# Kernel optimization log

Hardware: AMD Instinct MI355X
Metric: run time of the kernel (lower is better)

The kernel has to match this reference:

```python
import jax, jax.numpy as jnp
import numpy as np

N_NODES = 50000
N_EDGES = 800000
N_GRAPHS = 64
HEADS = 4
IN_CH, HID_CH, OUT_CH = 128, 64, 32


def setup_inputs() -> dict:
    key = jax.random.key(0)
    ks = jax.random.split(key, 13)
    x = jax.random.normal(ks[0], (N_NODES, IN_CH), dtype=jnp.float32)
    edge_index = jax.random.randint(ks[1], (2, N_EDGES), 0, N_NODES, dtype=jnp.int64)
    tensor_batch = jnp.sort(jax.random.randint(ks[2], (N_NODES,), 0, N_GRAPHS, dtype=jnp.int64))
    s = 0.1
    return {
        "x": x,
        "edge_index": edge_index,
        "tensor_batch": tensor_batch,
        "W1": jax.random.normal(ks[3], (IN_CH, HEADS * HID_CH), dtype=jnp.float32) * s,
        "a_src1": jax.random.normal(ks[4], (HEADS, HID_CH), dtype=jnp.float32) * s,
        "a_dst1": jax.random.normal(ks[5], (HEADS, HID_CH), dtype=jnp.float32) * s,
        "b1": jnp.zeros((HEADS * HID_CH,), dtype=jnp.float32),
        "W2": jax.random.normal(ks[6], (HEADS * HID_CH, HEADS * OUT_CH), dtype=jnp.float32) * s,
        "a_src2": jax.random.normal(ks[7], (HEADS, OUT_CH), dtype=jnp.float32) * s,
        "a_dst2": jax.random.normal(ks[8], (HEADS, OUT_CH), dtype=jnp.float32) * s,
        "b2": jnp.zeros((HEADS * OUT_CH,), dtype=jnp.float32),
        "Wout": jax.random.normal(ks[9], (HEADS * OUT_CH, 2), dtype=jnp.float32) * s,
        "bout": jnp.zeros((2,), dtype=jnp.float32),
    }


def gat_conv(x, src, dst, W, a_src, a_dst, b, heads, ch):
    """PyG-style GATConv (eval mode, self-loops already appended)."""
    N = x.shape[0]
    h = (x @ W).reshape(N, heads, ch)            # [N,H,C] per-head projection
    s = jnp.sum(h * a_src, axis=-1)              # [N,H] source attention term
    d = jnp.sum(h * a_dst, axis=-1)              # [N,H] dest attention term
    e = jax.nn.leaky_relu(s[src] + d[dst], negative_slope=0.2)   # [E,H]
    # segment softmax over incoming edges of each destination node
    m = jax.ops.segment_max(e, dst, num_segments=N)              # [N,H]
    ex = jnp.exp(e - m[dst])
    denom = jax.ops.segment_sum(ex, dst, num_segments=N)         # [N,H]
    alpha = ex / (denom[dst] + 1e-16)                            # [E,H]
    out = jax.ops.segment_sum(h[src] * alpha[:, :, None], dst, num_segments=N)
    return out.reshape(N, heads * ch) + b


def reference(x, edge_index, tensor_batch, W1, a_src1, a_dst1, b1,
              W2, a_src2, a_dst2, b2, Wout, bout):
    N = x.shape[0]
    loop = jnp.arange(N, dtype=edge_index.dtype)
    src = jnp.concatenate([edge_index[0], loop])  # add self-loops (PyG default)
    dst = jnp.concatenate([edge_index[1], loop])
    h = jax.nn.relu(gat_conv(x, src, dst, W1, a_src1, a_dst1, b1, HEADS, HID_CH))
    h = jax.nn.relu(gat_conv(h, src, dst, W2, a_src2, a_dst2, b2, HEADS, OUT_CH))
    # global mean pool per graph
    sums = jax.ops.segment_sum(h, tensor_batch, num_segments=N_GRAPHS)
    counts = jax.ops.segment_sum(jnp.ones((N, 1), h.dtype), tensor_batch, num_segments=N_GRAPHS)
    pooled = sums / jnp.maximum(counts, 1.0)
    logits = pooled @ Wout + bout
    return jax.nn.softmax(logits, axis=-1)
```

## Files before the change

### kernel.cpp

```cpp
#include <hip/hip_runtime.h>
#include <hip/hip_bf16.h>

#define N_NODES 50000
#define N_EDGES 800000
#define N_GRAPHS 64
#define HEADS 4
#define IN_CH 128
#define HID 64
#define F1 256
#define OUT_CH 32
#define F2 128
#define POOL_SPLITS 16
#define SCAN_B 256
#define SCAN_NB ((N_NODES + SCAN_B - 1) / SCAN_B)
#define GEMM_GRID ((N_NODES + 127) / 128)
#define COUNT_GRID ((N_EDGES + 255) / 256)

typedef unsigned short ushortT;
typedef unsigned int uintT;
typedef short v8s __attribute__((ext_vector_type(8)));
typedef float v4f __attribute__((ext_vector_type(4)));

__device__ __forceinline__ ushortT f2bf(float f) {
    union { float f; unsigned int i; } v; v.f = f;
    unsigned int x = v.i;
    unsigned int r = (x + 0x7fffu + ((x >> 16) & 1u)) >> 16;
    return (ushortT)r;
}
__device__ __forceinline__ float bf_lo(uintT w) {
    union { unsigned int i; float f; } v; v.i = w << 16; return v.f;
}
__device__ __forceinline__ float bf_hi(uintT w) {
    union { unsigned int i; float f; } v; v.i = w & 0xffff0000u; return v.f;
}

template <int FIN, int FOUT, bool ABF16>
__device__ __forceinline__ void gemm_body(const void* __restrict__ A,
                                          const float* __restrict__ W,
                                          const float* __restrict__ ASrc,
                                          const float* __restrict__ ADst,
                                          ushortT* __restrict__ out,
                                          float* __restrict__ s_out_g,
                                          float* __restrict__ d_out_g,
                                          int nrows, int bid) {
    constexpr int KC = FIN / 32;
    constexpr int NT = FOUT / 16;
    constexpr int NTH = (FOUT / HEADS) / 16;
    __shared__ uintT lW[FIN * FOUT / 2];
    int tid = threadIdx.x;
    constexpr int NQ = FIN * FOUT / 8;
    for (int i = tid; i < NQ; i += 256) {
        int lane = i & 63, g = i >> 6;
        int kc = g % KC, nt = g / KC;
        int n = nt * 16 + (lane & 15);
        int kbase = kc * 32 + (lane >> 4) * 8;
        union { uint4 q; ushortT u[8]; } pk;
#pragma unroll
        for (int j = 0; j < 8; j++) pk.u[j] = f2bf(W[(kbase + j) * FOUT + n]);
        ((uint4*)lW)[i] = pk.q;
    }
    __syncthreads();

    int wave = tid >> 6, lane = tid & 63;
    long rowA = (long)bid * 128 + wave * 32;
    long rowB = rowA + 16;
    bool doA = rowA < nrows, doB = rowB < nrows;
    if (!doA) return;
    int m = lane & 15, b = lane >> 4;

    v8s afA[KC], afB[KC];
    if (ABF16) {
        const ushortT* Ab = (const ushortT*)A;
#pragma unroll
        for (int kc = 0; kc < KC; kc++) {
            union { v8s v; uint4 q; } u;
            u.q = *(const uint4*)(Ab + (rowA + m) * FIN + kc * 32 + b * 8);
            afA[kc] = u.v;
            if (doB) {
                u.q = *(const uint4*)(Ab + (rowB + m) * FIN + kc * 32 + b * 8);
                afB[kc] = u.v;
            }
        }
    } else {
        const float* Af = (const float*)A;
#pragma unroll
        for (int kc = 0; kc < KC; kc++) {
            union { v8s v; ushortT u[8]; } u;
            const float* p = Af + (rowA + m) * FIN + kc * 32 + b * 8;
#pragma unroll
            for (int j = 0; j < 8; j++) u.u[j] = f2bf(p[j]);
            afA[kc] = u.v;
            if (doB) {
                const float* q = Af + (rowB + m) * FIN + kc * 32 + b * 8;
#pragma unroll
                for (int j = 0; j < 8; j++) u.u[j] = f2bf(q[j]);
                afB[kc] = u.v;
            }
        }
    }

    float spA[4] = {0,0,0,0}, dpA[4] = {0,0,0,0};
    float spB[4] = {0,0,0,0}, dpB[4] = {0,0,0,0};
    float skA[4], dkA[4], skB[4], dkB[4];
    const ushortT* lWs = (const ushortT*)lW;
#pragma unroll
    for (int nt = 0; nt < NT; nt++) {
        v4f cA = {0.f, 0.f, 0.f, 0.f}, cB = {0.f, 0.f, 0.f, 0.f};
#pragma unroll
        for (int kc = 0; kc < KC; kc++) {
            union { v8s v; uint4 q; } bu;
            bu.q = *(const uint4*)(lWs + ((nt * KC + kc) * 64 + lane) * 8);
            cA = __builtin_amdgcn_mfma_f32_16x16x32_bf16(afA[kc], bu.v, cA, 0, 0, 0);
            if (doB)
                cB = __builtin_amdgcn_mfma_f32_16x16x32_bf16(afB[kc], bu.v, cB, 0, 0, 0);
        }
        int col = nt * 16 + m;
        float av = ASrc[col], dv = ADst[col];
        long rA = rowA + b * 4;
#pragma unroll
        for (int reg = 0; reg < 4; reg++) {
            out[(rA + reg) * FOUT + col] = f2bf(cA[reg]);
            spA[reg] += cA[reg] * av;
            dpA[reg] += cA[reg] * dv;
        }
        if (doB) {
            long rB = rowB + b * 4;
#pragma unroll
            for (int reg = 0; reg < 4; reg++) {
                out[(rB + reg) * FOUT + col] = f2bf(cB[reg]);
                spB[reg] += cB[reg] * av;
                dpB[reg] += cB[reg] * dv;
            }
        }
        if ((nt % NTH) == NTH - 1) {
#pragma unroll
            for (int o = 1; o < 16; o <<= 1) {
#pragma unroll
                for (int reg = 0; reg < 4; reg++) {
                    spA[reg] += __shfl_xor(spA[reg], o, 64);
                    dpA[reg] += __shfl_xor(dpA[reg], o, 64);
                    spB[reg] += __shfl_xor(spB[reg], o, 64);
                    dpB[reg] += __shfl_xor(dpB[reg], o, 64);
                }
            }
            int hd = nt / NTH;
#pragma unroll
            for (int reg = 0; reg < 4; reg++) {
                if (m == hd) {
                    skA[reg] = spA[reg]; dkA[reg] = dpA[reg];
                    skB[reg] = spB[reg]; dkB[reg] = dpB[reg];
                }
                spA[reg] = 0.f; dpA[reg] = 0.f;
                spB[reg] = 0.f; dpB[reg] = 0.f;
            }
        }
    }
    if (m < HEADS) {
        long rA = rowA + b * 4;
#pragma unroll
        for (int reg = 0; reg < 4; reg++) {
            s_out_g[(rA + reg) * HEADS + m] = skA[reg];
            d_out_g[(rA + reg) * HEADS + m] = dkA[reg];
        }
        if (doB) {
            long rB = rowB + b * 4;
#pragma unroll
            for (int reg = 0; reg < 4; reg++) {
                s_out_g[(rB + reg) * HEADS + m] = skB[reg];
                d_out_g[(rB + reg) * HEADS + m] = dkB[reg];
            }
        }
    }
}

__global__ __launch_bounds__(256) void k_mega1(
        const float* __restrict__ x, const float* __restrict__ W1,
        const float* __restrict__ asrc1, const float* __restrict__ adst1,
        ushortT* __restrict__ u_h, float* __restrict__ f_s, float* __restrict__ f_d,
        const int* __restrict__ ei, int* __restrict__ counts,
        int* __restrict__ rank) {
    if (blockIdx.x < GEMM_GRID) {
        gemm_body<IN_CH, F1, false>(x, W1, asrc1, adst1, u_h, f_s, f_d,
                                    N_NODES, blockIdx.x);
    } else {
        int e = (blockIdx.x - GEMM_GRID) * 256 + threadIdx.x;
        if (e < N_EDGES) {
            int dst = ei[N_EDGES + e];
            rank[e] = atomicAdd(&counts[dst], 1);
        }
    }
}

__global__ __launch_bounds__(256) void k_gemm2(
        const ushortT* __restrict__ A, const float* __restrict__ W2,
        const float* __restrict__ asrc2, const float* __restrict__ adst2,
        ushortT* __restrict__ u_h, float* __restrict__ f_s, float* __restrict__ f_d) {
    gemm_body<F1, F2, true>(A, W2, asrc2, adst2, u_h, f_s, f_d,
                            N_NODES, blockIdx.x);
}

__global__ void k_scan1(const int* __restrict__ counts, int* __restrict__ offs,
                        int* __restrict__ bsum) {
    __shared__ int sh[SCAN_B];
    int b = blockIdx.x, t = threadIdx.x;
    int i = b * SCAN_B + t;
    int v = (i < N_NODES) ? counts[i] : 0;
    sh[t] = v;
    __syncthreads();
    for (int o = 1; o < SCAN_B; o <<= 1) {
        int add = (t >= o) ? sh[t - o] : 0;
        __syncthreads();
        sh[t] += add;
        __syncthreads();
    }
    if (i < N_NODES) offs[i] = sh[t] - v;
    if (t == SCAN_B - 1) bsum[b] = sh[t];
}

__global__ void k_scan2(const int* __restrict__ bsum, int* __restrict__ bbase,
                        int* __restrict__ offs, const int* __restrict__ batch,
                        int* __restrict__ bounds) {
    __shared__ int sh[SCAN_B];
    int t = threadIdx.x;
    int v = (t < SCAN_NB) ? bsum[t] : 0;
    sh[t] = v;
    __syncthreads();
    for (int o = 1; o < SCAN_B; o <<= 1) {
        int add = (t >= o) ? sh[t - o] : 0;
        __syncthreads();
        sh[t] += add;
        __syncthreads();
    }
    if (t < SCAN_NB) bbase[t] = sh[t] - v;
    if (t == SCAN_B - 1) offs[N_NODES] = sh[t];
    if (t <= N_GRAPHS) {
        int lo = 0, hi = N_NODES;
        while (lo < hi) {
            int mid = (lo + hi) >> 1;
            if (batch[mid] < t) lo = mid + 1; else hi = mid;
        }
        bounds[t] = lo;
    }
}

__global__ void k_scatter(const int* __restrict__ ei, const int* __restrict__ offs,
                          const int* __restrict__ bbase, const int* __restrict__ rank,
                          int* __restrict__ csr_src) {
    int e = blockIdx.x * blockDim.x + threadIdx.x;
    if (e >= N_EDGES) return;
    int src = ei[e], dst = ei[N_EDGES + e];
    int pos = offs[dst] + bbase[dst >> 8] + rank[e];
    csr_src[pos] = src;
}

template <int H, int C, int VEC, bool OUT_BF16, int WPB, int CHUNK>
__global__ __launch_bounds__(64 * WPB) void k_agg(
        const ushortT* __restrict__ hb, const float* __restrict__ s,
        const float* __restrict__ d, const int* __restrict__ offs,
        const int* __restrict__ bbase, const int* __restrict__ csr_src,
        const float* __restrict__ bias, void* __restrict__ xout) {
    static_assert(H == 4, "H=4 assumed");
    constexpr int F = H * C;
    constexpr int TPN = F / VEC;
    static_assert(TPN == 64, "one wave per node");
    __shared__ int lsrc[WPB][CHUNK];
    __shared__ float lex[WPB][CHUNK * H];
    int wv = threadIdx.x >> 6;
    int n = blockIdx.x * WPB + wv;
    if (n >= N_NODES) return;
    int t = threadIdx.x & 63;
    int h = t / (C / VEC);
    int beg = offs[n] + bbase[n >> 8];
    int np1 = n + 1;
    int end = (np1 < N_NODES) ? offs[np1] + bbase[np1 >> 8] : offs[N_NODES];
    float4 dn = *(const float4*)(d + n * 4);

    const uint2* hb2 = (const uint2*)hb;
    const uintT* hb1 = (const uintT*)hb;

    float4 svn = *(const float4*)(s + n * 4);
    float ssel = (h == 0) ? svn.x : (h == 1) ? svn.y : (h == 2) ? svn.z : svn.w;
    float dsel = (h == 0) ? dn.x : (h == 1) ? dn.y : (h == 2) ? dn.z : dn.w;
    float es = ssel + dsel; es = es > 0.f ? es : 0.2f * es;
    float exs = __expf(es);
    float sumex = exs;
    float acc[VEC];
    if (VEC == 4) {
        uint2 w = hb2[(long)n * TPN + t];
        acc[0] = exs * bf_lo(w.x); acc[1] = exs * bf_hi(w.x);
        acc[2] = exs * bf_lo(w.y); acc[3] = exs * bf_hi(w.y);
    } else {
        uintT w = hb1[(long)n * TPN + t];
        acc[0] = exs * bf_lo(w); acc[1] = exs * bf_hi(w);
    }

    for (int base = beg; base < end; base += CHUNK) {
        int cnt = min(CHUNK, end - base);
        for (int i = t; i < cnt; i += 64) {
            int sn = csr_src[base + i];
            lsrc[wv][i] = sn;
            float4 sv = *(const float4*)(s + sn * 4);
            float e0 = sv.x + dn.x; e0 = e0 > 0.f ? e0 : 0.2f * e0;
            float e1 = sv.y + dn.y; e1 = e1 > 0.f ? e1 : 0.2f * e1;
            float e2 = sv.z + dn.z; e2 = e2 > 0.f ? e2 : 0.2f * e2;
            float e3 = sv.w + dn.w; e3 = e3 > 0.f ? e3 : 0.2f * e3;
            float4 exv = { __expf(e0), __expf(e1), __expf(e2), __expf(e3) };
            *(float4*)&lex[wv][i * 4] = exv;
        }
        asm volatile("s_waitcnt lgkmcnt(0)" ::: "memory");
#pragma unroll 4
        for (int i = 0; i < cnt; i++) {
            float ex = lex[wv][i * H + h];
            int sn = lsrc[wv][i];
            sumex += ex;
            if (VEC == 4) {
                uint2 w = hb2[(long)sn * TPN + t];
                acc[0] += ex * bf_lo(w.x);
                acc[1] += ex * bf_hi(w.x);
                acc[2] += ex * bf_lo(w.y);
                acc[3] += ex * bf_hi(w.y);
            } else {
                uintT w = hb1[(long)sn * TPN + t];
                acc[0] += ex * bf_lo(w);
                acc[1] += ex * bf_hi(w);
            }
        }
        asm volatile("" ::: "memory");
    }
    float inv = 1.f / (sumex + 1e-16f);
    float o[VEC];
#pragma unroll
    for (int j = 0; j < VEC; j++)
        o[j] = fmaxf(acc[j] * inv + bias[t * VEC + j], 0.f);
    if (OUT_BF16) {
        if (VEC == 4) {
            uint2 pk;
            pk.x = (uintT)f2bf(o[0]) | ((uintT)f2bf(o[1]) << 16);
            pk.y = (uintT)f2bf(o[2]) | ((uintT)f2bf(o[3]) << 16);
            ((uint2*)xout)[(long)n * TPN + t] = pk;
        } else {
            uintT pk = (uintT)f2bf(o[0]) | ((uintT)f2bf(o[1]) << 16);
            ((uintT*)xout)[(long)n * TPN + t] = pk;
        }
    } else {
        float* xo = (float*)xout;
#pragma unroll
        for (int j = 0; j < VEC; j++) xo[(long)n * F + t * VEC + j] = o[j];
    }
}

__global__ void k_pool_partial(const ushortT* __restrict__ x2, const int* __restrict__ bounds,
                               float* __restrict__ partial) {
    int g = blockIdx.x, s = blockIdx.y;
    int t = threadIdx.x;
    int n0 = bounds[g], n1 = bounds[g + 1];
    int len = n1 - n0;
    int a = n0 + (int)((long)len * s / POOL_SPLITS);
    int b = n0 + (int)((long)len * (s + 1) / POOL_SPLITS);
    float acc = 0.f;
    for (int n = a; n < b; n++) acc += bf_lo((uintT)x2[(long)n * F2 + t]);
    partial[((long)g * POOL_SPLITS + s) * F2 + t] = acc;
}

__global__ void k_head(const float* __restrict__ partial, const int* __restrict__ bounds,
                       const float* __restrict__ Wout, const float* __restrict__ bout,
                       float* __restrict__ out) {
    __shared__ float red0[F2], red1[F2];
    int g = blockIdx.x;
    int t = threadIdx.x;
    int cntN = bounds[g + 1] - bounds[g];
    float cnt = fmaxf((float)cntN, 1.0f);
    float sum = 0.f;
    for (int s = 0; s < POOL_SPLITS; s++)
        sum += partial[((long)g * POOL_SPLITS + s) * F2 + t];
    float p = sum / cnt;
    red0[t] = p * Wout[t * 2 + 0];
    red1[t] = p * Wout[t * 2 + 1];
    __syncthreads();
    for (int off = F2 / 2; off > 0; off >>= 1) {
        if (t < off) { red0[t] += red0[t + off]; red1[t] += red1[t + off]; }
        __syncthreads();
    }
    if (t == 0) {
        float l0 = red0[0] + bout[0];
        float l1 = red1[0] + bout[1];
        float m = fmaxf(l0, l1);
        float e0 = __expf(l0 - m), e1 = __expf(l1 - m);
        float inv = 1.f / (e0 + e1);
        out[g * 2 + 0] = e0 * inv;
        out[g * 2 + 1] = e1 * inv;
    }
}

extern "C" void kernel_launch(void* const* d_in, const int* in_sizes, int n_in,
                              void* d_out, int out_size, void* d_ws, size_t ws_size,
                              hipStream_t stream) {
    const float* x     = (const float*)d_in[0];
    const int*   ei    = (const int*)d_in[1];
    const int*   batch = (const int*)d_in[2];
    const float* W1    = (const float*)d_in[3];
    const float* asrc1 = (const float*)d_in[4];
    const float* adst1 = (const float*)d_in[5];
    const float* b1    = (const float*)d_in[6];
    const float* W2    = (const float*)d_in[7];
    const float* asrc2 = (const float*)d_in[8];
    const float* adst2 = (const float*)d_in[9];
    const float* b2    = (const float*)d_in[10];
    const float* Wout  = (const float*)d_in[11];
    const float* bout  = (const float*)d_in[12];

    char* ws = (char*)d_ws;
    size_t off = 0;
    auto alloc = [&](size_t bytes) -> void* {
        void* p = ws + off;
        off += (bytes + 255) / 256 * 256;
        return p;
    };
    ushortT* u_h   = (ushortT*)alloc(sizeof(ushortT) * (size_t)N_NODES * F1);
    ushortT* u_x1  = (ushortT*)alloc(sizeof(ushortT) * (size_t)N_NODES * F1);
    ushortT* u_x2  = (ushortT*)alloc(sizeof(ushortT) * (size_t)N_NODES * F2);
    float*   f_s   = (float*)alloc(sizeof(float) * (size_t)N_NODES * HEADS);
    float*   f_d   = (float*)alloc(sizeof(float) * (size_t)N_NODES * HEADS);
    int*     i_cnt = (int*)alloc(sizeof(int) * (size_t)N_NODES);
    int*     i_off = (int*)alloc(sizeof(int) * (size_t)(N_NODES + 1));
    int*     i_rnk = (int*)alloc(sizeof(int) * (size_t)N_EDGES);
    int*     i_csr = (int*)alloc(sizeof(int) * (size_t)N_EDGES);
    int*     i_bnd = (int*)alloc(sizeof(int) * (size_t)(N_GRAPHS + 1));
    int*     i_bs  = (int*)alloc(sizeof(int) * SCAN_NB);
    int*     i_bb  = (int*)alloc(sizeof(int) * SCAN_NB);
    float*   f_prt = (float*)alloc(sizeof(float) * (size_t)N_GRAPHS * POOL_SPLITS * F2);
    (void)ws_size; (void)in_sizes; (void)n_in; (void)out_size;

    hipMemsetAsync(i_cnt, 0, sizeof(int) * N_NODES, stream);

    k_mega1<<<GEMM_GRID + COUNT_GRID, 256, 0, stream>>>(
        x, W1, asrc1, adst1, u_h, f_s, f_d, ei, i_cnt, i_rnk);

    k_scan1<<<SCAN_NB, SCAN_B, 0, stream>>>(i_cnt, i_off, i_bs);
    k_scan2<<<1, SCAN_B, 0, stream>>>(i_bs, i_bb, i_off, batch, i_bnd);
    k_scatter<<<COUNT_GRID, 256, 0, stream>>>(ei, i_off, i_bb, i_rnk, i_csr);

    int agg_grid = (N_NODES + 3) / 4;

    k_agg<HEADS, HID, 4, true, 4, 128><<<agg_grid, 256, 0, stream>>>(
        u_h, f_s, f_d, i_off, i_bb, i_csr, b1, u_x1);

    k_gemm2<<<GEMM_GRID, 256, 0, stream>>>(u_x1, W2, asrc2, adst2, u_h, f_s, f_d);
    k_agg<HEADS, OUT_CH, 2, true, 4, 128><<<agg_grid, 256, 0, stream>>>(
        u_h, f_s, f_d, i_off, i_bb, i_csr, b2, u_x2);

    dim3 pgrid(N_GRAPHS, POOL_SPLITS);
    k_pool_partial<<<pgrid, F2, 0, stream>>>(u_x2, i_bnd, f_prt);
    k_head<<<N_GRAPHS, F2, 0, stream>>>(f_prt, i_bnd, Wout, bout, (float*)d_out);
}
```

Baseline: 294.6 us.

## Store projected features in fp8 and prepack weights and input to bf16

The GEMMs now write the projected node features h as fp8 instead of bf16, which halves the bytes the edge aggregation kernels gather per neighbour. A new pre-pass kernel converts x to bf16 and packs W1/W2 into the MFMA layout once, so GEMM blocks only copy prepacked weights into LDS. This lowers precision of the gathered features and adds an extra kernel launch plus a write and re-read of a bf16 copy of x.

```diff
diff --git a/kernel.cpp b/kernel.cpp
--- a/kernel.cpp
+++ b/kernel.cpp
@@ -15,11 +15,13 @@
 #define SCAN_NB ((N_NODES + SCAN_B - 1) / SCAN_B)
 #define GEMM_GRID ((N_NODES + 127) / 128)
 #define COUNT_GRID ((N_EDGES + 255) / 256)
+#define XPACK_GRID (N_NODES * IN_CH / 8 / 256)
 
 typedef unsigned short ushortT;
 typedef unsigned int uintT;
 typedef short v8s __attribute__((ext_vector_type(8)));
 typedef float v4f __attribute__((ext_vector_type(4)));
+typedef float v2f __attribute__((ext_vector_type(2)));
 
 __device__ __forceinline__ ushortT f2bf(float f) {
     union { float f; unsigned int i; } v; v.f = f;
@@ -33,32 +35,62 @@
 __device__ __forceinline__ float bf_hi(uintT w) {
     union { unsigned int i; float f; } v; v.i = w & 0xffff0000u; return v.f;
 }
-
-template <int FIN, int FOUT, bool ABF16>
-__device__ __forceinline__ void gemm_body(const void* __restrict__ A,
-                                          const float* __restrict__ W,
+__device__ __forceinline__ unsigned char f2fp8(float f) {
+    return (unsigned char)__builtin_amdgcn_cvt_pk_fp8_f32(f, f, 0u, false);
+}
+
+__device__ __forceinline__ void packW_one(const float* __restrict__ W,
+                                          uint4* __restrict__ dst,
+                                          int i, int FIN, int FOUT) {
+    int KC = FIN / 32;
+    int lane = i & 63, g = i >> 6;
+    int kc = g % KC, nt = g / KC;
+    int n = nt * 16 + (lane & 15);
+    int kbase = kc * 32 + (lane >> 4) * 8;
+    union { uint4 q; ushortT u[8]; } pk;
+#pragma unroll
+    for (int j = 0; j < 8; j++) pk.u[j] = f2bf(W[(kbase + j) * FOUT + n]);
+    dst[i] = pk.q;
+}
+
+__global__ __launch_bounds__(256) void k_pack(
+        const float* __restrict__ x, const float* __restrict__ W1,
+        const float* __restrict__ W2, uint4* __restrict__ wpk,
+        ushortT* __restrict__ xb) {
+    int b = blockIdx.x;
+    if (b < 32) {
+        int i = b * 256 + threadIdx.x;
+        if (i < 4096) packW_one(W1, wpk, i, IN_CH, F1);
+        else          packW_one(W2, wpk + 4096, i - 4096, F1, F2);
+    } else {
+        long i = (long)(b - 32) * 256 + threadIdx.x;
+        const float4* xf = (const float4*)x + i * 2;
+        float4 a = xf[0], c = xf[1];
+        union { uint4 q; ushortT u[8]; } pk;
+        pk.u[0] = f2bf(a.x); pk.u[1] = f2bf(a.y);
+        pk.u[2] = f2bf(a.z); pk.u[3] = f2bf(a.w);
+        pk.u[4] = f2bf(c.x); pk.u[5] = f2bf(c.y);
+        pk.u[6] = f2bf(c.z); pk.u[7] = f2bf(c.w);
+        ((uint4*)xb)[i] = pk.q;
+    }
+}
+
+template <int FIN, int FOUT>
+__device__ __forceinline__ void gemm_body(const ushortT* __restrict__ A,
+                                          const uint4* __restrict__ Wpk,
                                           const float* __restrict__ ASrc,
                                           const float* __restrict__ ADst,
-                                          ushortT* __restrict__ out,
+                                          unsigned char* __restrict__ out,
                                           float* __restrict__ s_out_g,
                                           float* __restrict__ d_out_g,
                                           int nrows, int bid) {
     constexpr int KC = FIN / 32;
     constexpr int NT = FOUT / 16;
     constexpr int NTH = (FOUT / HEADS) / 16;
-    __shared__ uintT lW[FIN * FOUT / 2];
+    constexpr int NQ = FIN * FOUT / 8;
+    __shared__ uint4 lW4[NQ];
     int tid = threadIdx.x;
-    constexpr int NQ = FIN * FOUT / 8;
-    for (int i = tid; i < NQ; i += 256) {
-        int lane = i & 63, g = i >> 6;
-        int kc = g % KC, nt = g / KC;
-        int n = nt * 16 + (lane & 15);
-        int kbase = kc * 32 + (lane >> 4) * 8;
-        union { uint4 q; ushortT u[8]; } pk;
-#pragma unroll
-        for (int j = 0; j < 8; j++) pk.u[j] = f2bf(W[(kbase + j) * FOUT + n]);
-        ((uint4*)lW)[i] = pk.q;
-    }
+    for (int i = tid; i < NQ; i += 256) lW4[i] = Wpk[i];
     __syncthreads();
 
     int wave = tid >> 6, lane = tid & 63;
@@ -69,40 +101,21 @@
     int m = lane & 15, b = lane >> 4;
 
     v8s afA[KC], afB[KC];
-    if (ABF16) {
-        const ushortT* Ab = (const ushortT*)A;
-#pragma unroll
-        for (int kc = 0; kc < KC; kc++) {
-            union { v8s v; uint4 q; } u;
-            u.q = *(const uint4*)(Ab + (rowA + m) * FIN + kc * 32 + b * 8);
-            afA[kc] = u.v;
-            if (doB) {
-                u.q = *(const uint4*)(Ab + (rowB + m) * FIN + kc * 32 + b * 8);
-                afB[kc] = u.v;
-            }
-        }
-    } else {
-        const float* Af = (const float*)A;
-#pragma unroll
-        for (int kc = 0; kc < KC; kc++) {
-            union { v8s v; ushortT u[8]; } u;
-            const float* p = Af + (rowA + m) * FIN + kc * 32 + b * 8;
-#pragma unroll
-            for (int j = 0; j < 8; j++) u.u[j] = f2bf(p[j]);
-            afA[kc] = u.v;
-            if (doB) {
-                const float* q = Af + (rowB + m) * FIN + kc * 32 + b * 8;
-#pragma unroll
-                for (int j = 0; j < 8; j++) u.u[j] = f2bf(q[j]);
-                afB[kc] = u.v;
-            }
+#pragma unroll
+    for (int kc = 0; kc < KC; kc++) {
+        union { v8s v; uint4 q; } u;
+        u.q = *(const uint4*)(A + (rowA + m) * FIN + kc * 32 + b * 8);
+        afA[kc] = u.v;
+        if (doB) {
+            u.q = *(const uint4*)(A + (rowB + m) * FIN + kc * 32 + b * 8);
+            afB[kc] = u.v;
         }
     }
 
     float spA[4] = {0,0,0,0}, dpA[4] = {0,0,0,0};
     float spB[4] = {0,0,0,0}, dpB[4] = {0,0,0,0};
     float skA[4], dkA[4], skB[4], dkB[4];
-    const ushortT* lWs = (const ushortT*)lW;
+    const ushortT* lWs = (const ushortT*)lW4;
 #pragma unroll
     for (int nt = 0; nt < NT; nt++) {
         v4f cA = {0.f, 0.f, 0.f, 0.f}, cB = {0.f, 0.f, 0.f, 0.f};
@@ -119,7 +132,7 @@
         long rA = rowA + b * 4;
 #pragma unroll
         for (int reg = 0; reg < 4; reg++) {
-            out[(rA + reg) * FOUT + col] = f2bf(cA[reg]);
+            out[(rA + reg) * FOUT + col] = f2fp8(cA[reg]);
             spA[reg] += cA[reg] * av;
             dpA[reg] += cA[reg] * dv;
         }
@@ -127,7 +140,7 @@
             long rB = rowB + b * 4;
 #pragma unroll
             for (int reg = 0; reg < 4; reg++) {
-                out[(rB + reg) * FOUT + col] = f2bf(cB[reg]);
+                out[(rB + reg) * FOUT + col] = f2fp8(cB[reg]);
                 spB[reg] += cB[reg] * av;
                 dpB[reg] += cB[reg] * dv;
             }
@@ -174,14 +187,14 @@
 }
 
 __global__ __launch_bounds__(256) void k_mega1(
-        const float* __restrict__ x, const float* __restrict__ W1,
+        const ushortT* __restrict__ xb, const uint4* __restrict__ wpk,
         const float* __restrict__ asrc1, const float* __restrict__ adst1,
-        ushortT* __restrict__ u_h, float* __restrict__ f_s, float* __restrict__ f_d,
-        const int* __restrict__ ei, int* __restrict__ counts,
-        int* __restrict__ rank) {
+        unsigned char* __restrict__ u_h, float* __restrict__ f_s,
+        float* __restrict__ f_d, const int* __restrict__ ei,
+        int* __restrict__ counts, int* __restrict__ rank) {
     if (blockIdx.x < GEMM_GRID) {
-        gemm_body<IN_CH, F1, false>(x, W1, asrc1, adst1, u_h, f_s, f_d,
-                                    N_NODES, blockIdx.x);
+        gemm_body<IN_CH, F1>(xb, wpk, asrc1, adst1, u_h, f_s, f_d,
+                             N_NODES, blockIdx.x);
     } else {
         int e = (blockIdx.x - GEMM_GRID) * 256 + threadIdx.x;
         if (e < N_EDGES) {
@@ -192,11 +205,12 @@
 }
 
 __global__ __launch_bounds__(256) void k_gemm2(
-        const ushortT* __restrict__ A, const float* __restrict__ W2,
+        const ushortT* __restrict__ A, const uint4* __restrict__ wpk2,
         const float* __restrict__ asrc2, const float* __restrict__ adst2,
-        ushortT* __restrict__ u_h, float* __restrict__ f_s, float* __restrict__ f_d) {
-    gemm_body<F1, F2, true>(A, W2, asrc2, adst2, u_h, f_s, f_d,
-                            N_NODES, blockIdx.x);
+        unsigned char* __restrict__ u_h, float* __restrict__ f_s,
+        float* __restrict__ f_d) {
+    gemm_body<F1, F2>(A, wpk2, asrc2, adst2, u_h, f_s, f_d,
+                      N_NODES, blockIdx.x);
 }
 
 __global__ void k_scan1(const int* __restrict__ counts, int* __restrict__ offs,
@@ -253,12 +267,12 @@
     csr_src[pos] = src;
 }
 
-template <int H, int C, int VEC, bool OUT_BF16, int WPB, int CHUNK>
+template <int H, int C, int VEC, int WPB, int CHUNK>
 __global__ __launch_bounds__(64 * WPB) void k_agg(
-        const ushortT* __restrict__ hb, const float* __restrict__ s,
+        const unsigned char* __restrict__ hb, const float* __restrict__ s,
         const float* __restrict__ d, const int* __restrict__ offs,
         const int* __restrict__ bbase, const int* __restrict__ csr_src,
-        const float* __restrict__ bias, void* __restrict__ xout) {
+        const float* __restrict__ bias, ushortT* __restrict__ xout) {
     static_assert(H == 4, "H=4 assumed");
     constexpr int F = H * C;
     constexpr int TPN = F / VEC;
@@ -275,8 +289,8 @@
     int end = (np1 < N_NODES) ? offs[np1] + bbase[np1 >> 8] : offs[N_NODES];
     float4 dn = *(const float4*)(d + n * 4);
 
-    const uint2* hb2 = (const uint2*)hb;
-    const uintT* hb1 = (const uintT*)hb;
+    const uintT* hb4 = (const uintT*)hb;
+    const ushortT* hb2s = (const ushortT*)hb;
 
     float4 svn = *(const float4*)(s + n * 4);
     float ssel = (h == 0) ? svn.x : (h == 1) ? svn.y : (h == 2) ? svn.z : svn.w;
@@ -286,12 +300,15 @@
     float sumex = exs;
     float acc[VEC];
     if (VEC == 4) {
-        uint2 w = hb2[(long)n * TPN + t];
-        acc[0] = exs * bf_lo(w.x); acc[1] = exs * bf_hi(w.x);
-        acc[2] = exs * bf_lo(w.y); acc[3] = exs * bf_hi(w.y);
+        uintT w = hb4[(long)n * TPN + t];
+        v2f p0 = __builtin_amdgcn_cvt_pk_f32_fp8(w, false);
+        v2f p1 = __builtin_amdgcn_cvt_pk_f32_fp8(w, true);
+        acc[0] = exs * p0.x; acc[1] = exs * p0.y;
+        acc[2] = exs * p1.x; acc[3] = exs * p1.y;
     } else {
-        uintT w = hb1[(long)n * TPN + t];
-        acc[0] = exs * bf_lo(w); acc[1] = exs * bf_hi(w);
+        uintT w = hb2s[(long)n * TPN + t];
+        v2f p0 = __builtin_amdgcn_cvt_pk_f32_fp8(w, false);
+        acc[0] = exs * p0.x; acc[1] = exs * p0.y;
     }
 
     for (int base = beg; base < end; base += CHUNK) {
@@ -314,15 +331,18 @@
             int sn = lsrc[wv][i];
             sumex += ex;
             if (VEC == 4) {
-                uint2 w = hb2[(long)sn * TPN + t];
-                acc[0] += ex * bf_lo(w.x);
-                acc[1] += ex * bf_hi(w.x);
-                acc[2] += ex * bf_lo(w.y);
-                acc[3] += ex * bf_hi(w.y);
+                uintT w = hb4[(long)sn * TPN + t];
+                v2f p0 = __builtin_amdgcn_cvt_pk_f32_fp8(w, false);
+                v2f p1 = __builtin_amdgcn_cvt_pk_f32_fp8(w, true);
+                acc[0] += ex * p0.x;
+                acc[1] += ex * p0.y;
+                acc[2] += ex * p1.x;
+                acc[3] += ex * p1.y;
             } else {
-                uintT w = hb1[(long)sn * TPN + t];
-                acc[0] += ex * bf_lo(w);
-                acc[1] += ex * bf_hi(w);
+                uintT w = hb2s[(long)sn * TPN + t];
+                v2f p0 = __builtin_amdgcn_cvt_pk_f32_fp8(w, false);
+                acc[0] += ex * p0.x;
+                acc[1] += ex * p0.y;
             }
         }
         asm volatile("" ::: "memory");
@@ -332,20 +352,14 @@
 #pragma unroll
     for (int j = 0; j < VEC; j++)
         o[j] = fmaxf(acc[j] * inv + bias[t * VEC + j], 0.f);
-    if (OUT_BF16) {
-        if (VEC == 4) {
-            uint2 pk;
-            pk.x = (uintT)f2bf(o[0]) | ((uintT)f2bf(o[1]) << 16);
-            pk.y = (uintT)f2bf(o[2]) | ((uintT)f2bf(o[3]) << 16);
-            ((uint2*)xout)[(long)n * TPN + t] = pk;
-        } else {
-            uintT pk = (uintT)f2bf(o[0]) | ((uintT)f2bf(o[1]) << 16);
-            ((uintT*)xout)[(long)n * TPN + t] = pk;
-        }
+    if (VEC == 4) {
+        uint2 pk;
+        pk.x = (uintT)f2bf(o[0]) | ((uintT)f2bf(o[1]) << 16);
+        pk.y = (uintT)f2bf(o[2]) | ((uintT)f2bf(o[3]) << 16);
+        ((uint2*)xout)[(long)n * TPN + t] = pk;
     } else {
-        float* xo = (float*)xout;
-#pragma unroll
-        for (int j = 0; j < VEC; j++) xo[(long)n * F + t * VEC + j] = o[j];
+        uintT pk = (uintT)f2bf(o[0]) | ((uintT)f2bf(o[1]) << 16);
+        ((uintT*)xout)[(long)n * TPN + t] = pk;
     }
 }
 
@@ -416,9 +430,11 @@
         off += (bytes + 255) / 256 * 256;
         return p;
     };
-    ushortT* u_h   = (ushortT*)alloc(sizeof(ushortT) * (size_t)N_NODES * F1);
+    unsigned char* u_h = (unsigned char*)alloc((size_t)N_NODES * F1);
     ushortT* u_x1  = (ushortT*)alloc(sizeof(ushortT) * (size_t)N_NODES * F1);
     ushortT* u_x2  = (ushortT*)alloc(sizeof(ushortT) * (size_t)N_NODES * F2);
+    ushortT* xb    = (ushortT*)alloc(sizeof(ushortT) * (size_t)N_NODES * IN_CH);
+    uint4*   wpk   = (uint4*)alloc(sizeof(uint4) * 8192);
     float*   f_s   = (float*)alloc(sizeof(float) * (size_t)N_NODES * HEADS);
     float*   f_d   = (float*)alloc(sizeof(float) * (size_t)N_NODES * HEADS);
     int*     i_cnt = (int*)alloc(sizeof(int) * (size_t)N_NODES);
@@ -433,8 +449,10 @@
 
     hipMemsetAsync(i_cnt, 0, sizeof(int) * N_NODES, stream);
 
+    k_pack<<<32 + XPACK_GRID, 256, 0, stream>>>(x, W1, W2, wpk, xb);
+
     k_mega1<<<GEMM_GRID + COUNT_GRID, 256, 0, stream>>>(
-        x, W1, asrc1, adst1, u_h, f_s, f_d, ei, i_cnt, i_rnk);
+        xb, wpk, asrc1, adst1, u_h, f_s, f_d, ei, i_cnt, i_rnk);
 
     k_scan1<<<SCAN_NB, SCAN_B, 0, stream>>>(i_cnt, i_off, i_bs);
     k_scan2<<<1, SCAN_B, 0, stream>>>(i_bs, i_bb, i_off, batch, i_bnd);
@@ -442,11 +460,12 @@
 
     int agg_grid = (N_NODES + 3) / 4;
 
-    k_agg<HEADS, HID, 4, true, 4, 128><<<agg_grid, 256, 0, stream>>>(
+    k_agg<HEADS, HID, 4, 4, 128><<<agg_grid, 256, 0, stream>>>(
         u_h, f_s, f_d, i_off, i_bb, i_csr, b1, u_x1);
 
-    k_gemm2<<<GEMM_GRID, 256, 0, stream>>>(u_x1, W2, asrc2, adst2, u_h, f_s, f_d);
-    k_agg<HEADS, OUT_CH, 2, true, 4, 128><<<agg_grid, 256, 0, stream>>>(
+    k_gemm2<<<GEMM_GRID, 256, 0, stream>>>(u_x1, wpk + 4096, asrc2, adst2,
+                                           u_h, f_s, f_d);
+    k_agg<HEADS, OUT_CH, 2, 4, 128><<<agg_grid, 256, 0, stream>>>(
         u_h, f_s, f_d, i_off, i_bb, i_csr, b2, u_x2);
 
     dim3 pgrid(N_GRAPHS, POOL_SPLITS);
```

New measurement: 277.9 us. -5.7%, faster.
